# Performance work log

Measured on AMD Instinct MI355X. Metric: run time of the kernel, lower is better.

## Reference

```python
import jax, jax.numpy as jnp
import numpy as np

N = 50000          # num nodes
E_RAND = 1_600_000 # random edges (self-loops appended -> E = E_RAND + N)
H, D = 4, 32       # heads, per-head dim
HID = H * D        # 128
L = 3              # num GATv2 layers
NODE_DIM, GRAPH_DIM = 64, 32
EPS = 1e-5


def setup_inputs() -> dict:
    key = jax.random.key(0)
    ks = jax.random.split(key, 24)
    s = 0.05  # param init scale
    node_feats = jax.random.normal(ks[0], (N, NODE_DIM), jnp.float32)
    graph_feats = jax.random.normal(ks[1], (GRAPH_DIM,), jnp.float32)
    # random edges + self loops (mirrors dgl.add_self_loop in forward)
    src = jnp.concatenate([jax.random.randint(ks[2], (E_RAND,), 0, N), jnp.arange(N)]).astype(jnp.int32)
    dst = jnp.concatenate([jax.random.randint(ks[3], (E_RAND,), 0, N), jnp.arange(N)]).astype(jnp.int32)
    p = lambda k, shp: s * jax.random.normal(k, shp, jnp.float32)
    return {
        'node_feats': node_feats, 'graph_feats': graph_feats, 'src': src, 'dst': dst,
        'W_in': p(ks[4], (NODE_DIM, HID)), 'b_in': jnp.zeros((HID,), jnp.float32),
        'W_g': p(ks[5], (GRAPH_DIM, HID)), 'b_g': jnp.zeros((HID,), jnp.float32),
        'W_src': p(ks[6], (L, HID, HID)), 'b_src': jnp.zeros((L, HID), jnp.float32),
        'W_dst': p(ks[7], (L, HID, HID)), 'b_dst': jnp.zeros((L, HID), jnp.float32),
        'attn': p(ks[8], (L, H, D)),
        'ln_g': jnp.ones((L, HID), jnp.float32), 'ln_b': jnp.zeros((L, HID), jnp.float32),
        'W_f1': p(ks[9], (2 * HID, HID)), 'b_f1': jnp.zeros((HID,), jnp.float32),
        'W_f2': p(ks[10], (HID, HID)), 'b_f2': jnp.zeros((HID,), jnp.float32),
    }


def _layernorm(x, g, b):
    m = jnp.mean(x, -1, keepdims=True)
    v = jnp.mean(jnp.square(x - m), -1, keepdims=True)
    return (x - m) * jax.lax.rsqrt(v + EPS) * g + b


def _gatv2(h, src, dst, Ws, bs, Wd, bd, a):
    # DGL GATv2Conv (share_weights=False, residual identity since in==H*D)
    fs = (h @ Ws + bs).reshape(N, H, D)
    fd = (h @ Wd + bd).reshape(N, H, D)
    e = jax.nn.leaky_relu(fs[src] + fd[dst], 0.2)          # [E,H,D]
    logits = jnp.einsum('ehd,hd->eh', e, a)                # [E,H]
    mx = jax.ops.segment_max(logits, dst, num_segments=N)  # [N,H]
    ex = jnp.exp(logits - mx[dst])
    den = jax.ops.segment_sum(ex, dst, num_segments=N)     # [N,H]
    alpha = ex / den[dst]                                  # edge softmax
    out = jax.ops.segment_sum(alpha[:, :, None] * fs[src], dst, num_segments=N)
    return out.reshape(N, HID) + h                         # identity residual


def reference(node_feats, graph_feats, src, dst, W_in, b_in, W_g, b_g,
              W_src, b_src, W_dst, b_dst, attn, ln_g, ln_b,
              W_f1, b_f1, W_f2, b_f2):
    h = node_feats @ W_in + b_in                # [N,HID]
    graph_h = graph_feats @ W_g + b_g           # [HID]
    for l in range(L):
        h_new = _gatv2(h, src, dst, W_src[l], b_src[l], W_dst[l], b_dst[l], attn[l])
        h = jax.nn.relu(_layernorm(h + h_new, ln_g[l], ln_b[l]))  # dropout eval-mode
    pooled = jnp.mean(h, axis=0)                # [HID]
    combined = jnp.concatenate([pooled, graph_h])
    graph_emb = jax.nn.relu(combined @ W_f1 + b_f1) @ W_f2 + b_f2
    return graph_emb, h
```

## Files before the change

### kernel.cpp

```cpp
#include <hip/hip_runtime.h>

typedef unsigned short ushort_t;
typedef unsigned int   uint_t;
typedef unsigned char  uchar_t;
typedef __attribute__((ext_vector_type(8))) __bf16 bf16x8;
typedef __attribute__((ext_vector_type(4))) float   f32x4;

__device__ __forceinline__ float bl(uint_t u){ return __uint_as_float(u<<16); }
__device__ __forceinline__ float bh(uint_t u){ return __uint_as_float(u & 0xffff0000u); }
__device__ __forceinline__ ushort_t f2b(float f){
  uint_t x = __float_as_uint(f);
  return (ushort_t)((x + 0x7fffu + ((x>>16)&1u)) >> 16);
}
__device__ __forceinline__ uint_t pack2(float a, float b){
  return (uint_t)f2b(a) | ((uint_t)f2b(b) << 16);
}

#define NBK 128
#define PBLK 256

__global__ void k_zero(int* __restrict__ p, int n){
  int i = blockIdx.x*256 + threadIdx.x;
  if (i < n) p[i] = 0;
}

__global__ __launch_bounds__(256) void k_hist_bucket(
    const int* __restrict__ dst, int* __restrict__ bhist, int E, int epb)
{
  __shared__ int lh[NBK];
  int blk = blockIdx.x, t = threadIdx.x;
  if (t < NBK) lh[t] = 0;
  __syncthreads();
  int s = blk*epb, e = s + epb; if (e > E) e = E;
  for (int i = s + t; i < e; i += 256)
    atomicAdd(&lh[dst[i] >> 9], 1);
  __syncthreads();
  if (t < NBK) bhist[t*PBLK + blk] = lh[t];
}

__global__ __launch_bounds__(1024) void k_scan2(
    const int* __restrict__ bhist, int* __restrict__ gOff,
    int* __restrict__ bucketOff, int E)
{
  __shared__ int sums[1024];
  int tid = threadIdx.x;
  int s0 = tid * 32;
  int local = 0;
  #pragma unroll
  for (int i = 0; i < 32; ++i) local += bhist[s0 + i];
  sums[tid] = local;
  __syncthreads();
  for (int off = 1; off < 1024; off <<= 1) {
    int v = (tid >= off) ? sums[tid - off] : 0;
    __syncthreads();
    sums[tid] += v;
    __syncthreads();
  }
  int run = (tid == 0) ? 0 : sums[tid - 1];
  #pragma unroll
  for (int i = 0; i < 32; ++i) { gOff[s0 + i] = run; run += bhist[s0 + i]; }
  __syncthreads();
  if (tid < NBK) bucketOff[tid] = gOff[tid*PBLK];
  if (tid == NBK) bucketOff[NBK] = E;
}

__global__ __launch_bounds__(256) void k_part(
    const int* __restrict__ src, const int* __restrict__ dst,
    const int* __restrict__ gOff, uint_t* __restrict__ part, int E, int epb)
{
  __shared__ int loff[NBK];
  int blk = blockIdx.x, t = threadIdx.x;
  if (t < NBK) loff[t] = gOff[t*PBLK + blk];
  __syncthreads();
  int s = blk*epb, e = s + epb; if (e > E) e = E;
  for (int i = s + t; i < e; i += 256) {
    int d = dst[i];
    int b = d >> 9;
    int p = atomicAdd(&loff[b], 1);
    part[p] = (uint_t)src[i] | ((uint_t)(d & 511) << 16);
  }
}

__global__ __launch_bounds__(512) void k_csr(
    const uint_t* __restrict__ part, const int* __restrict__ bucketOff,
    int* __restrict__ rowp, int* __restrict__ csrc32, int N, int E)
{
  __shared__ int lcnt[512];
  __shared__ int lpos[512];
  int b = blockIdx.x, t = threadIdx.x;
  int base = b << 9;
  int cnt = N - base; if (cnt > 512) cnt = 512;
  lcnt[t] = 0;
  __syncthreads();
  int s = bucketOff[b], e = bucketOff[b + 1];
  for (int i = s + t; i < e; i += 512)
    atomicAdd(&lcnt[part[i] >> 16], 1);
  __syncthreads();
  int v = lcnt[t];
  lpos[t] = v;
  __syncthreads();
  for (int off = 1; off < 512; off <<= 1) {
    int u = (t >= off) ? lpos[t - off] : 0;
    __syncthreads();
    lpos[t] += u;
    __syncthreads();
  }
  int rp = s + lpos[t] - v;
  if (t < cnt) rowp[base + t] = rp;
  if (b == 0 && t == 0) rowp[N] = E;
  __syncthreads();
  lpos[t] = rp;
  __syncthreads();
  for (int i = s + t; i < e; i += 512) {
    uint_t pr = part[i];
    int p = atomicAdd(&lpos[pr >> 16], 1);
    csrc32[p] = (int)((pr & 0xffffu) << 7);
  }
}

__global__ __launch_bounds__(256) void k_gemm_in(
    const float* __restrict__ nf, const float* __restrict__ W,
    const float* __restrict__ b, ushort_t* __restrict__ HB, int N)
{
  __shared__ float sA[64*64];
  int row0 = blockIdx.x * 64;
  int tid = threadIdx.x;
  {
    int q = tid;
    #pragma unroll
    for (int j = 0; j < 4; ++j, q += 256) {
      int r = q >> 4;
      int c = (q & 15) << 2;
      float4 v = make_float4(0.f,0.f,0.f,0.f);
      if (row0 + r < N) v = *(const float4*)&nf[(size_t)(row0 + r)*64 + c];
      *(float4*)&sA[r*64 + c] = v;
    }
  }
  __syncthreads();
  int cg = tid & 15, rg = tid >> 4;
  int c0 = cg * 8;
  float acc[4][8];
  #pragma unroll
  for (int i = 0; i < 4; ++i)
    #pragma unroll
    for (int j = 0; j < 8; ++j) acc[i][j] = 0.f;
  for (int k = 0; k < 64; ++k) {
    float4 wa = *(const float4*)&W[k*128 + c0];
    float4 wb = *(const float4*)&W[k*128 + c0 + 4];
    float w[8] = {wa.x,wa.y,wa.z,wa.w,wb.x,wb.y,wb.z,wb.w};
    float hv[4];
    #pragma unroll
    for (int i = 0; i < 4; ++i) hv[i] = sA[(rg*4 + i)*64 + k];
    #pragma unroll
    for (int i = 0; i < 4; ++i)
      #pragma unroll
      for (int j = 0; j < 8; ++j) acc[i][j] += hv[i]*w[j];
  }
  float4 b1 = *(const float4*)&b[c0];
  float4 b2 = *(const float4*)&b[c0 + 4];
  float bb[8] = {b1.x,b1.y,b1.z,b1.w,b2.x,b2.y,b2.z,b2.w};
  #pragma unroll
  for (int i = 0; i < 4; ++i) {
    int row = row0 + rg*4 + i;
    if (row < N) {
      uint4 hb;
      hb.x = pack2(acc[i][0]+bb[0], acc[i][1]+bb[1]);
      hb.y = pack2(acc[i][2]+bb[2], acc[i][3]+bb[3]);
      hb.z = pack2(acc[i][4]+bb[4], acc[i][5]+bb[5]);
      hb.w = pack2(acc[i][6]+bb[6], acc[i][7]+bb[7]);
      *(uint4*)&HB[(size_t)row*128 + c0] = hb;
    }
  }
}

__global__ __launch_bounds__(256) void k_wswz(
    const float* __restrict__ Wsrc, const float* __restrict__ Wdst,
    ushort_t* __restrict__ WB)
{
  int t = blockIdx.x*256 + threadIdx.x;
  if (t >= 3*16*4*64) return;
  int l = t >> 12;
  int rem = t & 4095;
  int ct = rem >> 8;
  int kc = (rem >> 6) & 3;
  int lane = rem & 63;
  int n = ct*16 + (lane & 15);
  int kbase = kc*32 + (lane >> 4)*8;
  const float* Wp; int nn;
  if (n < 128) { Wp = Wsrc + l*16384; nn = n; }
  else         { Wp = Wdst + l*16384; nn = n - 128; }
  uint4 o;
  o.x = pack2(Wp[(kbase+0)*128+nn], Wp[(kbase+1)*128+nn]);
  o.y = pack2(Wp[(kbase+2)*128+nn], Wp[(kbase+3)*128+nn]);
  o.z = pack2(Wp[(kbase+4)*128+nn], Wp[(kbase+5)*128+nn]);
  o.w = pack2(Wp[(kbase+6)*128+nn], Wp[(kbase+7)*128+nn]);
  *(uint4*)&WB[(size_t)t * 8] = o;
}

__global__ __launch_bounds__(256) void k_gemm_mfma(
    const ushort_t* __restrict__ HB, const ushort_t* __restrict__ WB,
    const float* __restrict__ bsrc, const float* __restrict__ bdst,
    uchar_t* __restrict__ FS8, ushort_t* __restrict__ FD, int N)
{
  int m0 = blockIdx.x * 32;
  int tid = threadIdx.x;
  int w = tid >> 6, lane = tid & 63;
  int lrow = lane & 15, lk = lane >> 4;

  bf16x8 a[2][4];
  #pragma unroll
  for (int rt = 0; rt < 2; ++rt) {
    int row = m0 + rt*16 + lrow;
    if (row > N-1) row = N-1;
    #pragma unroll
    for (int kc = 0; kc < 4; ++kc)
      a[rt][kc] = *(const bf16x8*)&HB[(size_t)row*128 + kc*32 + lk*8];
  }

  #pragma unroll
  for (int c = 0; c < 4; ++c) {
    int ct = w*4 + c;
    int n = ct*16 + lrow;
    bf16x8 bfr[4];
    #pragma unroll
    for (int kc = 0; kc < 4; ++kc)
      bfr[kc] = *(const bf16x8*)&WB[((size_t)(ct*4 + kc)*64 + lane) * 8];
    if (ct < 8) {
      float bias = bsrc[n];
      #pragma unroll
      for (int rt = 0; rt < 2; ++rt) {
        f32x4 acc = {0.f, 0.f, 0.f, 0.f};
        #pragma unroll
        for (int kc = 0; kc < 4; ++kc)
          acc = __builtin_amdgcn_mfma_f32_16x16x32_bf16(a[rt][kc], bfr[kc], acc, 0, 0, 0);
        int r = m0 + rt*16 + lk*4;
        int w01 = __builtin_amdgcn_cvt_pk_fp8_f32(acc[0]+bias, acc[1]+bias, 0, false);
        int w23 = __builtin_amdgcn_cvt_pk_fp8_f32(acc[2]+bias, acc[3]+bias, 0, false);
        if (r     < N) FS8[(size_t)(r    )*128 + n] = (uchar_t)(w01);
        if (r + 1 < N) FS8[(size_t)(r + 1)*128 + n] = (uchar_t)(w01 >> 8);
        if (r + 2 < N) FS8[(size_t)(r + 2)*128 + n] = (uchar_t)(w23);
        if (r + 3 < N) FS8[(size_t)(r + 3)*128 + n] = (uchar_t)(w23 >> 8);
      }
    } else {
      int nn = n & 127;
      float bias = bdst[nn];
      #pragma unroll
      for (int rt = 0; rt < 2; ++rt) {
        f32x4 acc = {0.f, 0.f, 0.f, 0.f};
        #pragma unroll
        for (int kc = 0; kc < 4; ++kc)
          acc = __builtin_amdgcn_mfma_f32_16x16x32_bf16(a[rt][kc], bfr[kc], acc, 0, 0, 0);
        #pragma unroll
        for (int reg = 0; reg < 4; ++reg) {
          int row = m0 + rt*16 + lk*4 + reg;
          if (row < N) FD[(size_t)row*128 + nn] = f2b(acc[reg] + bias);
        }
      }
    }
  }
}

__global__ __launch_bounds__(256) void k_edge(
    const uchar_t* __restrict__ FS8, const ushort_t* __restrict__ FD,
    ushort_t* __restrict__ HB, float* __restrict__ H,
    const int* __restrict__ rowp, const int* __restrict__ csrc32,
    const float* __restrict__ attn, const float* __restrict__ lng,
    const float* __restrict__ lnb, int last, int N)
{
  int node = __builtin_amdgcn_readfirstlane(blockIdx.x * 4 + (threadIdx.x >> 6));
  if (node >= N) return;
  int lane = threadIdx.x & 63;
  int g = lane >> 4;
  int c = lane & 15;
  int cb = c << 3;

  float fdv[8], av[8];
  {
    uint4 fdu = *(const uint4*)((const char*)FD + node*256 + (cb << 1));
    fdv[0]=bl(fdu.x); fdv[1]=bh(fdu.x); fdv[2]=bl(fdu.y); fdv[3]=bh(fdu.y);
    fdv[4]=bl(fdu.z); fdv[5]=bh(fdu.z); fdv[6]=bl(fdu.w); fdv[7]=bh(fdu.w);
    float4 a1 = *(const float4*)&attn[cb];
    float4 a2 = *(const float4*)&attn[cb + 4];
    av[0]=a1.x*1.44269504f; av[1]=a1.y*1.44269504f;
    av[2]=a1.z*1.44269504f; av[3]=a1.w*1.44269504f;
    av[4]=a2.x*1.44269504f; av[5]=a2.y*1.44269504f;
    av[6]=a2.z*1.44269504f; av[7]=a2.w*1.44269504f;
  }
  int beg = __builtin_amdgcn_readfirstlane(rowp[node]);
  int end = __builtin_amdgcn_readfirstlane(rowp[node + 1]);
  int deg = end - beg;
  int nfull = deg >> 3, rem = deg & 7;
  int tb = beg + (nfull << 3);
  int endm1 = end - 1;

  float den = 0.f;
  float acc[8];
  #pragma unroll
  for (int k = 0; k < 8; ++k) acc[k] = 0.f;

  uint2 bA0, bA1, bB0, bB1, bT0, bT1;

  #define PREF8(b0, b1, kb) {                                               \
    int s0 = csrc32[(kb) + g];                                              \
    int s1 = csrc32[(kb) + 4 + g];                                          \
    b0 = *(const uint2*)((const char*)FS8 + s0 + cb);                       \
    b1 = *(const uint2*)((const char*)FS8 + s1 + cb);                       \
  }

  #define QMATH(u, MASKED, kbq) {                                           \
    float cf[8];                                                            \
    { auto p01 = __builtin_amdgcn_cvt_pk_f32_fp8((int)(u).x, false);        \
      auto p23 = __builtin_amdgcn_cvt_pk_f32_fp8((int)(u).x, true);         \
      auto p45 = __builtin_amdgcn_cvt_pk_f32_fp8((int)(u).y, false);        \
      auto p67 = __builtin_amdgcn_cvt_pk_f32_fp8((int)(u).y, true);         \
      cf[0]=p01[0]; cf[1]=p01[1]; cf[2]=p23[0]; cf[3]=p23[1];               \
      cf[4]=p45[0]; cf[5]=p45[1]; cf[6]=p67[0]; cf[7]=p67[1]; }             \
    float p = 0.f;                                                          \
    _Pragma("unroll")                                                       \
    for (int k = 0; k < 8; ++k) {                                           \
      float t = cf[k] + fdv[k]; t = fmaxf(t, 0.2f*t);                       \
      p += t * av[k];                                                       \
    }                                                                       \
    p += __shfl_xor(p, 1);                                                  \
    p += __shfl_xor(p, 2);                                                  \
    p += __shfl_xor(p, 4);                                                  \
    p += __shfl_xor(p, 8);                                                  \
    float ex = __builtin_amdgcn_exp2f(p);                                   \
    if (MASKED) ex = ((kbq) + g < end) ? ex : 0.f;                          \
    den += ex;                                                              \
    _Pragma("unroll")                                                       \
    for (int k = 0; k < 8; ++k) acc[k] += ex * cf[k];                       \
  }

  if (rem) {
    int i0 = tb + g;     i0 = (i0 < endm1) ? i0 : endm1;
    int i1 = tb + 4 + g; i1 = (i1 < endm1) ? i1 : endm1;
    int s0 = csrc32[i0];
    int s1 = csrc32[i1];
    bT0 = *(const uint2*)((const char*)FS8 + s0 + cb);
    bT1 = *(const uint2*)((const char*)FS8 + s1 + cb);
  }
  if (nfull) {
    PREF8(bA0, bA1, beg)
    int remaining = nfull, kb = beg + 8;
    for (;;) {
      if (remaining > 1) { PREF8(bB0, bB1, kb) }
      QMATH(bA0, 0, 0) QMATH(bA1, 0, 0)
      if (--remaining == 0) break;
      kb += 8;
      if (remaining > 1) { PREF8(bA0, bA1, kb) }
      QMATH(bB0, 0, 0) QMATH(bB1, 0, 0)
      if (--remaining == 0) break;
      kb += 8;
    }
  }
  if (rem) {
    QMATH(bT0, 1, tb)
    QMATH(bT1, 1, tb + 4)
  }
  #undef PREF8
  #undef QMATH

  den += __shfl_xor(den, 16); den += __shfl_xor(den, 32);
  #pragma unroll
  for (int k = 0; k < 8; ++k) {
    acc[k] += __shfl_xor(acc[k], 16);
    acc[k] += __shfl_xor(acc[k], 32);
  }
  float rden = 1.f / den;

  float x[8];
  {
    uint4 hu = *(const uint4*)((const char*)HB + node*256 + (cb << 1));
    float hb[8] = {bl(hu.x),bh(hu.x),bl(hu.y),bh(hu.y),
                   bl(hu.z),bh(hu.z),bl(hu.w),bh(hu.w)};
    #pragma unroll
    for (int k = 0; k < 8; ++k) x[k] = 2.f*hb[k] + acc[k]*rden;
  }
  float s = 0.f;
  #pragma unroll
  for (int k = 0; k < 8; ++k) s += x[k];
  s += __shfl_xor(s, 1); s += __shfl_xor(s, 2);
  s += __shfl_xor(s, 4); s += __shfl_xor(s, 8);
  float mean = s * (1.f/128.f);
  float v = 0.f;
  #pragma unroll
  for (int k = 0; k < 8; ++k) { x[k] -= mean; v += x[k]*x[k]; }
  v += __shfl_xor(v, 1); v += __shfl_xor(v, 2);
  v += __shfl_xor(v, 4); v += __shfl_xor(v, 8);
  float rs = rsqrtf(v * (1.f/128.f) + 1e-5f);
  float4 g1 = *(const float4*)&lng[cb];
  float4 g2 = *(const float4*)&lng[cb + 4];
  float4 be1 = *(const float4*)&lnb[cb];
  float4 be2 = *(const float4*)&lnb[cb + 4];
  float gv[8] = {g1.x,g1.y,g1.z,g1.w,g2.x,g2.y,g2.z,g2.w};
  float bv[8] = {be1.x,be1.y,be1.z,be1.w,be2.x,be2.y,be2.z,be2.w};
  float y[8];
  #pragma unroll
  for (int k = 0; k < 8; ++k) y[k] = fmaxf(x[k]*rs*gv[k] + bv[k], 0.f);

  if (lane < 16) {
    if (last) {
      float4 o1 = make_float4(y[0],y[1],y[2],y[3]);
      float4 o2 = make_float4(y[4],y[5],y[6],y[7]);
      *(float4*)((char*)H + node*512 + (cb << 2))      = o1;
      *(float4*)((char*)H + node*512 + (cb << 2) + 16) = o2;
    } else {
      uint4 o;
      o.x = pack2(y[0],y[1]); o.y = pack2(y[2],y[3]);
      o.z = pack2(y[4],y[5]); o.w = pack2(y[6],y[7]);
      *(uint4*)((char*)HB + node*256 + (cb << 1)) = o;
    }
  }
}

__global__ __launch_bounds__(128) void k_pool(const float* __restrict__ H,
                                              float* __restrict__ pooled, int N){
  int c = threadIdx.x;
  float s = 0.f;
  for (int r = blockIdx.x; r < N; r += gridDim.x) s += H[(size_t)r*128 + c];
  atomicAdd(&pooled[c], s);
}

__global__ __launch_bounds__(256) void k_final(
    const float* __restrict__ gf, const float* __restrict__ pooled,
    const float* __restrict__ Wg, const float* __restrict__ bg,
    const float* __restrict__ Wf1, const float* __restrict__ bf1,
    const float* __restrict__ Wf2, const float* __restrict__ bf2v,
    float* __restrict__ out, float inv_n)
{
  __shared__ float comb[256];
  __shared__ float t1[128];
  int tid = threadIdx.x;
  if (tid < 128) {
    comb[tid] = pooled[tid] * inv_n;
  } else {
    int c = tid - 128;
    float s = bg[c];
    for (int k = 0; k < 32; ++k) s += gf[k] * Wg[k*128 + c];
    comb[128 + c] = s;
  }
  __syncthreads();
  if (tid < 128) {
    float s = bf1[tid];
    for (int k = 0; k < 256; ++k) s += comb[k] * Wf1[k*128 + tid];
    t1[tid] = fmaxf(s, 0.f);
  }
  __syncthreads();
  if (tid < 128) {
    float s = bf2v[tid];
    for (int k = 0; k < 128; ++k) s += t1[k] * Wf2[k*128 + tid];
    out[tid] = s;
  }
}

extern "C" void kernel_launch(void* const* d_in, const int* in_sizes, int n_in,
                              void* d_out, int out_size, void* d_ws, size_t ws_size,
                              hipStream_t stream) {
  const float* node_feats = (const float*)d_in[0];
  const float* graph_feats= (const float*)d_in[1];
  const int*   src        = (const int*)d_in[2];
  const int*   dst        = (const int*)d_in[3];
  const float* W_in  = (const float*)d_in[4];
  const float* b_in  = (const float*)d_in[5];
  const float* W_g   = (const float*)d_in[6];
  const float* b_g   = (const float*)d_in[7];
  const float* W_src = (const float*)d_in[8];
  const float* b_src = (const float*)d_in[9];
  const float* W_dst = (const float*)d_in[10];
  const float* b_dst = (const float*)d_in[11];
  const float* attn  = (const float*)d_in[12];
  const float* ln_g  = (const float*)d_in[13];
  const float* ln_b  = (const float*)d_in[14];
  const float* W_f1  = (const float*)d_in[15];
  const float* b_f1  = (const float*)d_in[16];
  const float* W_f2  = (const float*)d_in[17];
  const float* b_f2  = (const float*)d_in[18];

  int N = in_sizes[0] / 64;
  int E = in_sizes[2];

  float* out_f = (float*)d_out;
  float* GEMB  = out_f;
  float* H     = out_f + 128;

  float*    pooled = (float*)d_ws;
  uchar_t*  FS8 = (uchar_t*)((char*)d_ws + 512);
  ushort_t* FD = (ushort_t*)(FS8 + (size_t)N * 128);
  ushort_t* HB = FD + (size_t)N * 128;
  ushort_t* WB = HB + (size_t)N * 128;
  int* ibase = (int*)(WB + 3*32768);
  int* rowp      = ibase;
  int* bhist     = ibase + N + 1;
  int* gOff      = bhist + NBK*PBLK;
  int* bucketOff = gOff + NBK*PBLK;
  int* csrc32    = bucketOff + NBK + 1;
  uint_t* part   = (uint_t*)FS8;

  int epb = (E + PBLK - 1) / PBLK;
  int nb  = (N + 511) >> 9;

  k_zero<<<1, 256, 0, stream>>>((int*)pooled, 128);

  k_wswz<<<(3*16*4*64 + 255)/256, 256, 0, stream>>>(W_src, W_dst, WB);
  k_hist_bucket<<<PBLK, 256, 0, stream>>>(dst, bhist, E, epb);
  k_scan2<<<1, 1024, 0, stream>>>(bhist, gOff, bucketOff, E);
  k_part<<<PBLK, 256, 0, stream>>>(src, dst, gOff, part, E, epb);
  k_csr<<<nb, 512, 0, stream>>>(part, bucketOff, rowp, csrc32, N, E);

  k_gemm_in<<<(N + 63)/64, 256, 0, stream>>>(node_feats, W_in, b_in, HB, N);

  for (int l = 0; l < 3; ++l) {
    k_gemm_mfma<<<(N + 31)/32, 256, 0, stream>>>(
        HB, WB + (size_t)l*32768, b_src + l*128, b_dst + l*128, FS8, FD, N);
    k_edge<<<(N + 3)/4, 256, 0, stream>>>(
        FS8, FD, HB, H, rowp, csrc32,
        attn + l*128, ln_g + l*128, ln_b + l*128, (l == 2) ? 1 : 0, N);
  }

  k_pool<<<512, 128, 0, stream>>>(H, pooled, N);
  k_final<<<1, 256, 0, stream>>>(graph_feats, pooled, W_g, b_g, W_f1, b_f1,
                                 W_f2, b_f2, GEMB, 1.0f / (float)N);
}
```

Measured before the change: 385.1 us.

## Fuse preprocessing kernels, unroll edge loop to 16, use DPP reductions and abs-form leaky ReLU

Merges the zero, weight-swizzle and histogram kernels into one launch, and the partition and input GEMM into another, cutting launch count and idle gaps. The edge kernel now processes 16 edges per step with deeper prefetch. Leaky ReLU times attention is rewritten as 0.6x+0.4|x| folded into scaled attention vectors using FMAs. Shuffle-based 16-lane reductions are replaced with DPP row reductions. The deeper prefetch raises register use, and the fused GEMM block carries the partition path's shared memory, both of which may lower occupancy.

```diff
diff --git a/kernel.cpp b/kernel.cpp
--- a/kernel.cpp
+++ b/kernel.cpp
@@ -16,26 +16,56 @@
   return (uint_t)f2b(a) | ((uint_t)f2b(b) << 16);
 }
 
+__device__ __forceinline__ float row_reduce16(float p){
+  float t;
+  t = __uint_as_float(__builtin_amdgcn_update_dpp(0, __float_as_uint(p), 0x121, 0xf, 0xf, true)); p += t;
+  t = __uint_as_float(__builtin_amdgcn_update_dpp(0, __float_as_uint(p), 0x122, 0xf, 0xf, true)); p += t;
+  t = __uint_as_float(__builtin_amdgcn_update_dpp(0, __float_as_uint(p), 0x124, 0xf, 0xf, true)); p += t;
+  t = __uint_as_float(__builtin_amdgcn_update_dpp(0, __float_as_uint(p), 0x128, 0xf, 0xf, true)); p += t;
+  return p;
+}
+
 #define NBK 128
 #define PBLK 256
 
-__global__ void k_zero(int* __restrict__ p, int n){
-  int i = blockIdx.x*256 + threadIdx.x;
-  if (i < n) p[i] = 0;
-}
-
-__global__ __launch_bounds__(256) void k_hist_bucket(
-    const int* __restrict__ dst, int* __restrict__ bhist, int E, int epb)
-{
-  __shared__ int lh[NBK];
-  int blk = blockIdx.x, t = threadIdx.x;
-  if (t < NBK) lh[t] = 0;
-  __syncthreads();
-  int s = blk*epb, e = s + epb; if (e > E) e = E;
-  for (int i = s + t; i < e; i += 256)
-    atomicAdd(&lh[dst[i] >> 9], 1);
-  __syncthreads();
-  if (t < NBK) bhist[t*PBLK + blk] = lh[t];
+__global__ __launch_bounds__(256) void k_fuse_a(
+    const float* __restrict__ Wsrc, const float* __restrict__ Wdst,
+    ushort_t* __restrict__ WB,
+    const int* __restrict__ dst, int* __restrict__ bhist, int E, int epb,
+    float* __restrict__ pooled)
+{
+  int blk = blockIdx.x;
+  if (blk < 48) {
+    int t = blk*256 + threadIdx.x;
+    int l = t >> 12;
+    int rem = t & 4095;
+    int ct = rem >> 8;
+    int kc = (rem >> 6) & 3;
+    int lane = rem & 63;
+    int n = ct*16 + (lane & 15);
+    int kbase = kc*32 + (lane >> 4)*8;
+    const float* Wp; int nn;
+    if (n < 128) { Wp = Wsrc + l*16384; nn = n; }
+    else         { Wp = Wdst + l*16384; nn = n - 128; }
+    uint4 o;
+    o.x = pack2(Wp[(kbase+0)*128+nn], Wp[(kbase+1)*128+nn]);
+    o.y = pack2(Wp[(kbase+2)*128+nn], Wp[(kbase+3)*128+nn]);
+    o.z = pack2(Wp[(kbase+4)*128+nn], Wp[(kbase+5)*128+nn]);
+    o.w = pack2(Wp[(kbase+6)*128+nn], Wp[(kbase+7)*128+nn]);
+    *(uint4*)&WB[(size_t)t * 8] = o;
+  } else if (blk < 304) {
+    __shared__ int lh[NBK];
+    int b2 = blk - 48, t = threadIdx.x;
+    if (t < NBK) lh[t] = 0;
+    __syncthreads();
+    int s = b2*epb, e = s + epb; if (e > E) e = E;
+    for (int i = s + t; i < e; i += 256)
+      atomicAdd(&lh[dst[i] >> 9], 1);
+    __syncthreads();
+    if (t < NBK) bhist[t*PBLK + b2] = lh[t];
+  } else {
+    if (threadIdx.x < 128) pooled[threadIdx.x] = 0.f;
+  }
 }
 
 __global__ __launch_bounds__(1024) void k_scan2(
@@ -64,20 +94,74 @@
   if (tid == NBK) bucketOff[NBK] = E;
 }
 
-__global__ __launch_bounds__(256) void k_part(
+__global__ __launch_bounds__(256) void k_fuse_b(
     const int* __restrict__ src, const int* __restrict__ dst,
-    const int* __restrict__ gOff, uint_t* __restrict__ part, int E, int epb)
+    const int* __restrict__ gOff, uint_t* __restrict__ part, int E, int epb,
+    const float* __restrict__ nf, const float* __restrict__ W,
+    const float* __restrict__ b, ushort_t* __restrict__ HB, int N)
 {
   __shared__ int loff[NBK];
-  int blk = blockIdx.x, t = threadIdx.x;
-  if (t < NBK) loff[t] = gOff[t*PBLK + blk];
-  __syncthreads();
-  int s = blk*epb, e = s + epb; if (e > E) e = E;
-  for (int i = s + t; i < e; i += 256) {
-    int d = dst[i];
-    int b = d >> 9;
-    int p = atomicAdd(&loff[b], 1);
-    part[p] = (uint_t)src[i] | ((uint_t)(d & 511) << 16);
+  __shared__ float sA[64*64];
+  if (blockIdx.x < PBLK) {
+    int blk = blockIdx.x, t = threadIdx.x;
+    if (t < NBK) loff[t] = gOff[t*PBLK + blk];
+    __syncthreads();
+    int s = blk*epb, e = s + epb; if (e > E) e = E;
+    for (int i = s + t; i < e; i += 256) {
+      int d = dst[i];
+      int bb = d >> 9;
+      int p = atomicAdd(&loff[bb], 1);
+      part[p] = (uint_t)src[i] | ((uint_t)(d & 511) << 16);
+    }
+  } else {
+    int row0 = (blockIdx.x - PBLK) * 64;
+    int tid = threadIdx.x;
+    {
+      int q = tid;
+      #pragma unroll
+      for (int j = 0; j < 4; ++j, q += 256) {
+        int r = q >> 4;
+        int c = (q & 15) << 2;
+        float4 v = make_float4(0.f,0.f,0.f,0.f);
+        if (row0 + r < N) v = *(const float4*)&nf[(size_t)(row0 + r)*64 + c];
+        *(float4*)&sA[r*64 + c] = v;
+      }
+    }
+    __syncthreads();
+    int cg = tid & 15, rg = tid >> 4;
+    int c0 = cg * 8;
+    float acc[4][8];
+    #pragma unroll
+    for (int i = 0; i < 4; ++i)
+      #pragma unroll
+      for (int j = 0; j < 8; ++j) acc[i][j] = 0.f;
+    for (int k = 0; k < 64; ++k) {
+      float4 wa = *(const float4*)&W[k*128 + c0];
+      float4 wb = *(const float4*)&W[k*128 + c0 + 4];
+      float w[8] = {wa.x,wa.y,wa.z,wa.w,wb.x,wb.y,wb.z,wb.w};
+      float hv[4];
+      #pragma unroll
+      for (int i = 0; i < 4; ++i) hv[i] = sA[(rg*4 + i)*64 + k];
+      #pragma unroll
+      for (int i = 0; i < 4; ++i)
+        #pragma unroll
+        for (int j = 0; j < 8; ++j) acc[i][j] += hv[i]*w[j];
+    }
+    float4 b1 = *(const float4*)&b[c0];
+    float4 b2 = *(const float4*)&b[c0 + 4];
+    float bb[8] = {b1.x,b1.y,b1.z,b1.w,b2.x,b2.y,b2.z,b2.w};
+    #pragma unroll
+    for (int i = 0; i < 4; ++i) {
+      int row = row0 + rg*4 + i;
+      if (row < N) {
+        uint4 hb;
+        hb.x = pack2(acc[i][0]+bb[0], acc[i][1]+bb[1]);
+        hb.y = pack2(acc[i][2]+bb[2], acc[i][3]+bb[3]);
+        hb.z = pack2(acc[i][4]+bb[4], acc[i][5]+bb[5]);
+        hb.w = pack2(acc[i][6]+bb[6], acc[i][7]+bb[7]);
+        *(uint4*)&HB[(size_t)row*128 + c0] = hb;
+      }
+    }
   }
 }
 
@@ -116,85 +200,6 @@
     int p = atomicAdd(&lpos[pr >> 16], 1);
     csrc32[p] = (int)((pr & 0xffffu) << 7);
   }
-}
-
-__global__ __launch_bounds__(256) void k_gemm_in(
-    const float* __restrict__ nf, const float* __restrict__ W,
-    const float* __restrict__ b, ushort_t* __restrict__ HB, int N)
-{
-  __shared__ float sA[64*64];
-  int row0 = blockIdx.x * 64;
-  int tid = threadIdx.x;
-  {
-    int q = tid;
-    #pragma unroll
-    for (int j = 0; j < 4; ++j, q += 256) {
-      int r = q >> 4;
-      int c = (q & 15) << 2;
-      float4 v = make_float4(0.f,0.f,0.f,0.f);
-      if (row0 + r < N) v = *(const float4*)&nf[(size_t)(row0 + r)*64 + c];
-      *(float4*)&sA[r*64 + c] = v;
-    }
-  }
-  __syncthreads();
-  int cg = tid & 15, rg = tid >> 4;
-  int c0 = cg * 8;
-  float acc[4][8];
-  #pragma unroll
-  for (int i = 0; i < 4; ++i)
-    #pragma unroll
-    for (int j = 0; j < 8; ++j) acc[i][j] = 0.f;
-  for (int k = 0; k < 64; ++k) {
-    float4 wa = *(const float4*)&W[k*128 + c0];
-    float4 wb = *(const float4*)&W[k*128 + c0 + 4];
-    float w[8] = {wa.x,wa.y,wa.z,wa.w,wb.x,wb.y,wb.z,wb.w};
-    float hv[4];
-    #pragma unroll
-    for (int i = 0; i < 4; ++i) hv[i] = sA[(rg*4 + i)*64 + k];
-    #pragma unroll
-    for (int i = 0; i < 4; ++i)
-      #pragma unroll
-      for (int j = 0; j < 8; ++j) acc[i][j] += hv[i]*w[j];
-  }
-  float4 b1 = *(const float4*)&b[c0];
-  float4 b2 = *(const float4*)&b[c0 + 4];
-  float bb[8] = {b1.x,b1.y,b1.z,b1.w,b2.x,b2.y,b2.z,b2.w};
-  #pragma unroll
-  for (int i = 0; i < 4; ++i) {
-    int row = row0 + rg*4 + i;
-    if (row < N) {
-      uint4 hb;
-      hb.x = pack2(acc[i][0]+bb[0], acc[i][1]+bb[1]);
-      hb.y = pack2(acc[i][2]+bb[2], acc[i][3]+bb[3]);
-      hb.z = pack2(acc[i][4]+bb[4], acc[i][5]+bb[5]);
-      hb.w = pack2(acc[i][6]+bb[6], acc[i][7]+bb[7]);
-      *(uint4*)&HB[(size_t)row*128 + c0] = hb;
-    }
-  }
-}
-
-__global__ __launch_bounds__(256) void k_wswz(
-    const float* __restrict__ Wsrc, const float* __restrict__ Wdst,
-    ushort_t* __restrict__ WB)
-{
-  int t = blockIdx.x*256 + threadIdx.x;
-  if (t >= 3*16*4*64) return;
-  int l = t >> 12;
-  int rem = t & 4095;
-  int ct = rem >> 8;
-  int kc = (rem >> 6) & 3;
-  int lane = rem & 63;
-  int n = ct*16 + (lane & 15);
-  int kbase = kc*32 + (lane >> 4)*8;
-  const float* Wp; int nn;
-  if (n < 128) { Wp = Wsrc + l*16384; nn = n; }
-  else         { Wp = Wdst + l*16384; nn = n - 128; }
-  uint4 o;
-  o.x = pack2(Wp[(kbase+0)*128+nn], Wp[(kbase+1)*128+nn]);
-  o.y = pack2(Wp[(kbase+2)*128+nn], Wp[(kbase+3)*128+nn]);
-  o.z = pack2(Wp[(kbase+4)*128+nn], Wp[(kbase+5)*128+nn]);
-  o.w = pack2(Wp[(kbase+6)*128+nn], Wp[(kbase+7)*128+nn]);
-  *(uint4*)&WB[(size_t)t * 8] = o;
 }
 
 __global__ __launch_bounds__(256) void k_gemm_mfma(
@@ -274,23 +279,25 @@
   int c = lane & 15;
   int cb = c << 3;
 
-  float fdv[8], av[8];
+  float fdv[8], av6[8], av4[8];
   {
     uint4 fdu = *(const uint4*)((const char*)FD + node*256 + (cb << 1));
     fdv[0]=bl(fdu.x); fdv[1]=bh(fdu.x); fdv[2]=bl(fdu.y); fdv[3]=bh(fdu.y);
     fdv[4]=bl(fdu.z); fdv[5]=bh(fdu.z); fdv[6]=bl(fdu.w); fdv[7]=bh(fdu.w);
     float4 a1 = *(const float4*)&attn[cb];
     float4 a2 = *(const float4*)&attn[cb + 4];
-    av[0]=a1.x*1.44269504f; av[1]=a1.y*1.44269504f;
-    av[2]=a1.z*1.44269504f; av[3]=a1.w*1.44269504f;
-    av[4]=a2.x*1.44269504f; av[5]=a2.y*1.44269504f;
-    av[6]=a2.z*1.44269504f; av[7]=a2.w*1.44269504f;
+    float aa[8] = {a1.x,a1.y,a1.z,a1.w,a2.x,a2.y,a2.z,a2.w};
+    #pragma unroll
+    for (int k = 0; k < 8; ++k) {
+      av6[k] = aa[k] * 0.865617024f;
+      av4[k] = aa[k] * 0.577078016f;
+    }
   }
   int beg = __builtin_amdgcn_readfirstlane(rowp[node]);
   int end = __builtin_amdgcn_readfirstlane(rowp[node + 1]);
   int deg = end - beg;
-  int nfull = deg >> 3, rem = deg & 7;
-  int tb = beg + (nfull << 3);
+  int npair = deg >> 4, ntail = deg & 15;
+  int tb = beg + (npair << 4);
   int endm1 = end - 1;
 
   float den = 0.f;
@@ -298,16 +305,23 @@
   #pragma unroll
   for (int k = 0; k < 8; ++k) acc[k] = 0.f;
 
-  uint2 bA0, bA1, bB0, bB1, bT0, bT1;
-
-  #define PREF8(b0, b1, kb) {                                               \
+  uint2 a0,a1q,a2q,a3q, b0,b1q,b2q,b3q, t0,t1q,t2q,t3q;
+
+  #define PREF(bu0, bu1, kb) {                                              \
     int s0 = csrc32[(kb) + g];                                              \
     int s1 = csrc32[(kb) + 4 + g];                                          \
-    b0 = *(const uint2*)((const char*)FS8 + s0 + cb);                       \
-    b1 = *(const uint2*)((const char*)FS8 + s1 + cb);                       \
-  }
-
-  #define QMATH(u, MASKED, kbq) {                                           \
+    bu0 = *(const uint2*)((const char*)FS8 + s0 + cb);                      \
+    bu1 = *(const uint2*)((const char*)FS8 + s1 + cb);                      \
+  }
+
+  #define PREFT(bu0, bu1, kb) {                                             \
+    int i0 = (kb) + g;     i0 = (i0 < endm1) ? i0 : endm1;                  \
+    int i1 = (kb) + 4 + g; i1 = (i1 < endm1) ? i1 : endm1;                  \
+    bu0 = *(const uint2*)((const char*)FS8 + csrc32[i0] + cb);              \
+    bu1 = *(const uint2*)((const char*)FS8 + csrc32[i1] + cb);              \
+  }
+
+  #define QM(u, MASKED, kbq) {                                              \
     float cf[8];                                                            \
     { auto p01 = __builtin_amdgcn_cvt_pk_f32_fp8((int)(u).x, false);        \
       auto p23 = __builtin_amdgcn_cvt_pk_f32_fp8((int)(u).x, true);         \
@@ -318,48 +332,39 @@
     float p = 0.f;                                                          \
     _Pragma("unroll")                                                       \
     for (int k = 0; k < 8; ++k) {                                           \
-      float t = cf[k] + fdv[k]; t = fmaxf(t, 0.2f*t);                       \
-      p += t * av[k];                                                       \
+      float x = cf[k] + fdv[k];                                             \
+      p = fmaf(x, av6[k], p);                                               \
+      p = fmaf(fabsf(x), av4[k], p);                                        \
     }                                                                       \
-    p += __shfl_xor(p, 1);                                                  \
-    p += __shfl_xor(p, 2);                                                  \
-    p += __shfl_xor(p, 4);                                                  \
-    p += __shfl_xor(p, 8);                                                  \
+    p = row_reduce16(p);                                                    \
     float ex = __builtin_amdgcn_exp2f(p);                                   \
     if (MASKED) ex = ((kbq) + g < end) ? ex : 0.f;                          \
     den += ex;                                                              \
     _Pragma("unroll")                                                       \
-    for (int k = 0; k < 8; ++k) acc[k] += ex * cf[k];                       \
-  }
-
-  if (rem) {
-    int i0 = tb + g;     i0 = (i0 < endm1) ? i0 : endm1;
-    int i1 = tb + 4 + g; i1 = (i1 < endm1) ? i1 : endm1;
-    int s0 = csrc32[i0];
-    int s1 = csrc32[i1];
-    bT0 = *(const uint2*)((const char*)FS8 + s0 + cb);
-    bT1 = *(const uint2*)((const char*)FS8 + s1 + cb);
-  }
-  if (nfull) {
-    PREF8(bA0, bA1, beg)
-    int remaining = nfull, kb = beg + 8;
+    for (int k = 0; k < 8; ++k) acc[k] = fmaf(ex, cf[k], acc[k]);           \
+  }
+
+  if (ntail) { PREFT(t0, t1q, tb) PREFT(t2q, t3q, tb + 8) }
+  if (npair) {
+    PREF(a0, a1q, beg) PREF(a2q, a3q, beg + 8)
+    int rem2 = npair, kb = beg + 16;
     for (;;) {
-      if (remaining > 1) { PREF8(bB0, bB1, kb) }
-      QMATH(bA0, 0, 0) QMATH(bA1, 0, 0)
-      if (--remaining == 0) break;
-      kb += 8;
-      if (remaining > 1) { PREF8(bA0, bA1, kb) }
-      QMATH(bB0, 0, 0) QMATH(bB1, 0, 0)
-      if (--remaining == 0) break;
-      kb += 8;
-    }
-  }
-  if (rem) {
-    QMATH(bT0, 1, tb)
-    QMATH(bT1, 1, tb + 4)
-  }
-  #undef PREF8
-  #undef QMATH
+      if (rem2 > 1) { PREF(b0, b1q, kb) PREF(b2q, b3q, kb + 8) }
+      QM(a0, 0, 0) QM(a1q, 0, 0) QM(a2q, 0, 0) QM(a3q, 0, 0)
+      if (--rem2 == 0) break;
+      kb += 16;
+      if (rem2 > 1) { PREF(a0, a1q, kb) PREF(a2q, a3q, kb + 8) }
+      QM(b0, 0, 0) QM(b1q, 0, 0) QM(b2q, 0, 0) QM(b3q, 0, 0)
+      if (--rem2 == 0) break;
+      kb += 16;
+    }
+  }
+  if (ntail) {
+    QM(t0, 1, tb) QM(t1q, 1, tb + 4) QM(t2q, 1, tb + 8) QM(t3q, 1, tb + 12)
+  }
+  #undef PREF
+  #undef PREFT
+  #undef QM
 
   den += __shfl_xor(den, 16); den += __shfl_xor(den, 32);
   #pragma unroll
@@ -380,14 +385,12 @@
   float s = 0.f;
   #pragma unroll
   for (int k = 0; k < 8; ++k) s += x[k];
-  s += __shfl_xor(s, 1); s += __shfl_xor(s, 2);
-  s += __shfl_xor(s, 4); s += __shfl_xor(s, 8);
+  s = row_reduce16(s);
   float mean = s * (1.f/128.f);
   float v = 0.f;
   #pragma unroll
   for (int k = 0; k < 8; ++k) { x[k] -= mean; v += x[k]*x[k]; }
-  v += __shfl_xor(v, 1); v += __shfl_xor(v, 2);
-  v += __shfl_xor(v, 4); v += __shfl_xor(v, 8);
+  v = row_reduce16(v);
   float rs = rsqrtf(v * (1.f/128.f) + 1e-5f);
   float4 g1 = *(const float4*)&lng[cb];
   float4 g2 = *(const float4*)&lng[cb + 4];
@@ -499,16 +502,13 @@
 
   int epb = (E + PBLK - 1) / PBLK;
   int nb  = (N + 511) >> 9;
-
-  k_zero<<<1, 256, 0, stream>>>((int*)pooled, 128);
-
-  k_wswz<<<(3*16*4*64 + 255)/256, 256, 0, stream>>>(W_src, W_dst, WB);
-  k_hist_bucket<<<PBLK, 256, 0, stream>>>(dst, bhist, E, epb);
+  int gemm_in_blocks = (N + 63) / 64;
+
+  k_fuse_a<<<305, 256, 0, stream>>>(W_src, W_dst, WB, dst, bhist, E, epb, pooled);
   k_scan2<<<1, 1024, 0, stream>>>(bhist, gOff, bucketOff, E);
-  k_part<<<PBLK, 256, 0, stream>>>(src, dst, gOff, part, E, epb);
+  k_fuse_b<<<PBLK + gemm_in_blocks, 256, 0, stream>>>(
+      src, dst, gOff, part, E, epb, node_feats, W_in, b_in, HB, N);
   k_csr<<<nb, 512, 0, stream>>>(part, bucketOff, rowp, csrc32, N, E);
-
-  k_gemm_in<<<(N + 63)/64, 256, 0, stream>>>(node_feats, W_in, b_in, HB, N);
 
   for (int l = 0; l < 3; ++l) {
     k_gemm_mfma<<<(N + 31)/32, 256, 0, stream>>>(
```

Result: faster. 352.9 us (-8.4%).
